# Kernel tuning notes

Measured on AMD Instinct MI355X. Metric: run time of the kernel, lower is better.

## Reference

```python
import jax, jax.numpy as jnp
import numpy as np

BATCH = 4096
N_AG = 32       # nodes (agents) per batch element
N_HE = 8        # hyperedges per batch element
F_IN = 256
F_OUT = 128
N_NODES = BATCH * N_AG
N_EDGES = BATCH * N_HE


def _build_incidence():
    # dense per-batch incidence (randn hyper_graph => all entries nonzero),
    # block-diagonal across the batch via index offsets
    b = jnp.arange(BATCH, dtype=jnp.int32)
    nodes = b[:, None, None] * N_AG + jnp.arange(N_AG, dtype=jnp.int32)[None, :, None]
    edges = b[:, None, None] * N_HE + jnp.arange(N_HE, dtype=jnp.int32)[None, None, :]
    node_idx = jnp.broadcast_to(nodes, (BATCH, N_AG, N_HE)).reshape(-1)
    edge_idx = jnp.broadcast_to(edges, (BATCH, N_AG, N_HE)).reshape(-1)
    return node_idx, edge_idx


def setup_inputs() -> dict:
    key = jax.random.key(0)
    k1, k2, k3 = jax.random.split(key, 3)
    inp = jax.random.normal(k1, (BATCH, N_AG, F_IN), jnp.float32)
    lin_w = jax.random.normal(k2, (F_IN, F_OUT), jnp.float32) * (1.0 / np.sqrt(F_IN))
    hgcn_bias = jnp.zeros((F_OUT,), jnp.float32)
    out_w = jax.random.normal(k3, (F_OUT, F_OUT), jnp.float32) * (1.0 / np.sqrt(F_OUT))
    out_b = jnp.zeros((F_OUT,), jnp.float32)
    node_idx, edge_idx = _build_incidence()
    return {"input": inp, "lin_w": lin_w, "hgcn_bias": hgcn_bias,
            "out_w": out_w, "out_b": out_b,
            "node_idx": node_idx, "edge_idx": edge_idx}


def reference(input, lin_w, hgcn_bias, out_w, out_b, node_idx, edge_idx):
    # X' = D^-1 H B^-1 H^T X Theta + bias, then Linear+ReLU output layer
    x = input.reshape(-1, F_IN) @ lin_w                       # [N, F_OUT]
    w = jnp.ones((N_EDGES,), x.dtype)                         # default hyperedge weights
    # node degree D (weighted by hyperedge weight) and edge degree B
    D = jax.ops.segment_sum(w[edge_idx], node_idx, num_segments=N_NODES)
    D_inv = jnp.where(D > 0, 1.0 / D, 0.0)
    deg = jax.ops.segment_sum(jnp.ones(edge_idx.shape, x.dtype), edge_idx,
                              num_segments=N_EDGES)
    B_inv = jnp.where(deg > 0, 1.0 / deg, 0.0)
    # propagate nodes -> hyperedges with norm B^-1 at target edges
    edge_feat = jax.ops.segment_sum(x[node_idx] * B_inv[edge_idx][:, None],
                                    edge_idx, num_segments=N_EDGES)   # [M, F_OUT]
    # propagate hyperedges -> nodes with norm D^-1 at target nodes
    out = jax.ops.segment_sum(edge_feat[edge_idx] * D_inv[node_idx][:, None],
                              node_idx, num_segments=N_NODES)         # [N, F_OUT]
    out = out + hgcn_bias
    return jax.nn.relu(out @ out_w + out_b)
```

## Files before the change

### kernel.cpp

```cpp
#include <hip/hip_runtime.h>


constexpr int BATCH = 4096;
constexpr int N_AG  = 32;
constexpr int F_IN  = 256;
constexpr int F_OUT = 128;
constexpr int G     = 8;

typedef float vfloat4 __attribute__((ext_vector_type(4)));
typedef float vfloat2 __attribute__((ext_vector_type(2)));

__global__ __launch_bounds__(512, 4) void hgcn_fused(
    const float* __restrict__ input,
    const float* __restrict__ lin_w,
    const float* __restrict__ bias1,
    const float* __restrict__ out_w,
    const float* __restrict__ bias2,
    float* __restrict__ out)
{
    const int t  = threadIdx.x;
    const int b0 = blockIdx.x * G;

    __shared__ __align__(16) float sm[G][F_IN];
    __shared__ __align__(16) float part[8][G][F_OUT];
    __shared__ __align__(16) float sh[G][F_OUT];
    __shared__ __align__(16) float sy[G][F_OUT];

    const int j2  = t & 63;
    const int oct = t >> 6;

    {
        const int g  = t >> 6;
        const int f4 = t & 63;
        const vfloat4* in4 = (const vfloat4*)input + (size_t)(b0 + g) * (N_AG * F_IN / 4);
        vfloat4 s = (vfloat4)0.f;
        #pragma unroll
        for (int a = 0; a < N_AG; ++a)
            s += __builtin_nontemporal_load(&in4[a * (F_IN / 4) + f4]);
        s *= (1.0f / 32.0f);
        *(vfloat4*)&sm[g][f4 * 4] = s;
    }
    __syncthreads();

    {
        const vfloat2* lw2 = (const vfloat2*)lin_w;
        const vfloat4* m4  = (const vfloat4*)&sm[0][0];
        vfloat2 acc[G];
        #pragma unroll
        for (int g = 0; g < G; ++g) acc[g] = (vfloat2)0.f;
        #pragma unroll 2
        for (int f4 = 0; f4 < 8; ++f4) {
            vfloat4 mm[G];
            #pragma unroll
            for (int g = 0; g < G; ++g)
                mm[g] = m4[g * (F_IN / 4) + oct * 8 + f4];
            #pragma unroll
            for (int c = 0; c < 4; ++c) {
                const int f = oct * 32 + f4 * 4 + c;
                vfloat2 wv = lw2[f * (F_OUT / 2) + j2];
                #pragma unroll
                for (int g = 0; g < G; ++g) {
                    acc[g].x += mm[g][c] * wv.x;
                    acc[g].y += mm[g][c] * wv.y;
                }
            }
        }
        #pragma unroll
        for (int g = 0; g < G; ++g)
            *(vfloat2*)&part[oct][g][j2 * 2] = acc[g];
    }
    __syncthreads();

    {
        const int g = t >> 6;
        const vfloat2* p2 = (const vfloat2*)&part[0][0][0];
        vfloat2 s = (vfloat2)0.f;
        #pragma unroll
        for (int o = 0; o < 8; ++o)
            s += p2[(o * G + g) * (F_OUT / 2) + j2];
        vfloat2 bb = ((const vfloat2*)bias1)[j2];
        s += bb;
        *(vfloat2*)&sh[g][j2 * 2] = s;
    }
    __syncthreads();

    {
        const vfloat2* ow2 = (const vfloat2*)out_w;
        const vfloat4* h4  = (const vfloat4*)&sh[0][0];
        vfloat2 acc[G];
        #pragma unroll
        for (int g = 0; g < G; ++g) acc[g] = (vfloat2)0.f;
        #pragma unroll 2
        for (int k4 = 0; k4 < 4; ++k4) {
            vfloat4 hh[G];
            #pragma unroll
            for (int g = 0; g < G; ++g)
                hh[g] = h4[g * (F_OUT / 4) + oct * 4 + k4];
            #pragma unroll
            for (int c = 0; c < 4; ++c) {
                const int k = oct * 16 + k4 * 4 + c;
                vfloat2 wv = ow2[k * (F_OUT / 2) + j2];
                #pragma unroll
                for (int g = 0; g < G; ++g) {
                    acc[g].x += hh[g][c] * wv.x;
                    acc[g].y += hh[g][c] * wv.y;
                }
            }
        }
        #pragma unroll
        for (int g = 0; g < G; ++g)
            *(vfloat2*)&part[oct][g][j2 * 2] = acc[g];
    }
    __syncthreads();

    {
        const int g = t >> 6;
        const vfloat2* p2 = (const vfloat2*)&part[0][0][0];
        vfloat2 s = (vfloat2)0.f;
        #pragma unroll
        for (int o = 0; o < 8; ++o)
            s += p2[(o * G + g) * (F_OUT / 2) + j2];
        vfloat2 bb = ((const vfloat2*)bias2)[j2];
        s += bb;
        vfloat2 yv;
        yv.x = s.x > 0.f ? s.x : 0.f;
        yv.y = s.y > 0.f ? s.y : 0.f;
        *(vfloat2*)&sy[g][j2 * 2] = yv;
    }
    __syncthreads();

    {
        const vfloat4* y4 = (const vfloat4*)&sy[0][0];
        const int col = t & 31;
        vfloat4 vy[G];
        #pragma unroll
        for (int g = 0; g < G; ++g) vy[g] = y4[g * 32 + col];
        vfloat4* o4 = (vfloat4*)out + (size_t)b0 * (N_AG * F_OUT / 4);
        #pragma unroll
        for (int r = 0; r < 16; ++r) {
            const int i = r * 512 + t;
            __builtin_nontemporal_store(vy[r >> 1], &o4[i]);
        }
    }
}

extern "C" void kernel_launch(void* const* d_in, const int* in_sizes, int n_in,
                              void* d_out, int out_size, void* d_ws, size_t ws_size,
                              hipStream_t stream) {
    const float* input = (const float*)d_in[0];
    const float* lin_w = (const float*)d_in[1];
    const float* b1    = (const float*)d_in[2];
    const float* out_w = (const float*)d_in[3];
    const float* b2    = (const float*)d_in[4];
    float* out = (float*)d_out;

    hgcn_fused<<<BATCH / G, 512, 0, stream>>>(input, lin_w, b1, out_w, b2, out);
}
```

Measured before the change: 214.8 us.

## Precompute fused weight matrix lin_w·out_w to collapse two GEMMs into one

A small pre-kernel multiplies lin_w by out_w, and folds bias1 through out_w and adds bias2, writing the product into workspace. The main kernel then runs one 256x128 matvec per group instead of two chained ones. This drops a stage, its barriers and the second weight read. The cost is an extra kernel launch each call, slightly different float rounding, and a fallback path that keeps the old kernel if workspace is too small.

```diff
diff --git a/kernel.cpp b/kernel.cpp
--- a/kernel.cpp
+++ b/kernel.cpp
@@ -10,24 +10,34 @@
 typedef float vfloat4 __attribute__((ext_vector_type(4)));
 typedef float vfloat2 __attribute__((ext_vector_type(2)));
 
-__global__ __launch_bounds__(512, 4) void hgcn_fused(
+__global__ __launch_bounds__(128) void fuse_weights(
+    const float* __restrict__ lin_w, const float* __restrict__ b1,
+    const float* __restrict__ out_w, const float* __restrict__ b2,
+    float* __restrict__ W, float* __restrict__ bf)
+{
+    const int j = threadIdx.x;
+    const int r = blockIdx.x;
+    const float* row = (r < F_IN) ? &lin_w[(size_t)r * F_OUT] : b1;
+    float acc = (r < F_IN) ? 0.f : b2[j];
+    #pragma unroll 8
+    for (int k = 0; k < F_OUT; ++k)
+        acc = fmaf(row[k], out_w[k * F_OUT + j], acc);
+    if (r < F_IN) W[r * F_OUT + j] = acc;
+    else          bf[j] = acc;
+}
+
+__global__ __launch_bounds__(512, 4) void hgcn_fusedw(
     const float* __restrict__ input,
-    const float* __restrict__ lin_w,
-    const float* __restrict__ bias1,
-    const float* __restrict__ out_w,
-    const float* __restrict__ bias2,
+    const float* __restrict__ W,
+    const float* __restrict__ bf,
     float* __restrict__ out)
 {
     const int t  = threadIdx.x;
     const int b0 = blockIdx.x * G;
 
     __shared__ __align__(16) float sm[G][F_IN];
-    __shared__ __align__(16) float part[8][G][F_OUT];
-    __shared__ __align__(16) float sh[G][F_OUT];
+    __shared__ __align__(16) float part[16][G][F_OUT];
     __shared__ __align__(16) float sy[G][F_OUT];
-
-    const int j2  = t & 63;
-    const int oct = t >> 6;
 
     {
         const int g  = t >> 6;
@@ -43,8 +53,87 @@
     __syncthreads();
 
     {
+        const int jq = t & 31, ks = t >> 5;
+        const vfloat4* W4 = (const vfloat4*)W;
+        const vfloat4* m4 = (const vfloat4*)&sm[0][0];
+        vfloat4 acc[G];
+        #pragma unroll
+        for (int g = 0; g < G; ++g) acc[g] = (vfloat4)0.f;
+        #pragma unroll
+        for (int f4 = 0; f4 < 4; ++f4) {
+            vfloat4 mm[G];
+            #pragma unroll
+            for (int g = 0; g < G; ++g)
+                mm[g] = m4[g * (F_IN / 4) + ks * 4 + f4];
+            #pragma unroll
+            for (int c = 0; c < 4; ++c) {
+                const int f = ks * 16 + f4 * 4 + c;
+                vfloat4 wv = W4[f * (F_OUT / 4) + jq];
+                #pragma unroll
+                for (int g = 0; g < G; ++g)
+                    acc[g] += mm[g][c] * wv;
+            }
+        }
+        #pragma unroll
+        for (int g = 0; g < G; ++g)
+            *(vfloat4*)&part[ks][g][jq * 4] = acc[g];
+    }
+    __syncthreads();
+
+    {
+        const int g = t >> 6, j2 = t & 63;
+        const vfloat2* p2 = (const vfloat2*)&part[0][0][0];
+        vfloat2 s = (vfloat2)0.f;
+        #pragma unroll
+        for (int ks = 0; ks < 16; ++ks)
+            s += p2[(ks * G + g) * (F_OUT / 2) + j2];
+        s += ((const vfloat2*)bf)[j2];
+        vfloat2 yv;
+        yv.x = s.x > 0.f ? s.x : 0.f;
+        yv.y = s.y > 0.f ? s.y : 0.f;
+        *(vfloat2*)&sy[g][j2 * 2] = yv;
+    }
+    __syncthreads();
+
+    {
+        const vfloat4* y4 = (const vfloat4*)&sy[0][0];
+        const int col = t & 31;
+        vfloat4 vy[G];
+        #pragma unroll
+        for (int g = 0; g < G; ++g) vy[g] = y4[g * 32 + col];
+        vfloat4* o4 = (vfloat4*)out + (size_t)b0 * (N_AG * F_OUT / 4);
+        #pragma unroll
+        for (int r = 0; r < 16; ++r)
+            __builtin_nontemporal_store(vy[r >> 1], &o4[r * 512 + t]);
+    }
+}
+
+__global__ __launch_bounds__(512, 4) void hgcn_fused_r3(
+    const float* __restrict__ input, const float* __restrict__ lin_w,
+    const float* __restrict__ bias1, const float* __restrict__ out_w,
+    const float* __restrict__ bias2, float* __restrict__ out)
+{
+    const int t = threadIdx.x;
+    const int b0 = blockIdx.x * G;
+    __shared__ __align__(16) float sm[G][F_IN];
+    __shared__ __align__(16) float part[8][G][F_OUT];
+    __shared__ __align__(16) float sh[G][F_OUT];
+    __shared__ __align__(16) float sy[G][F_OUT];
+    const int j2 = t & 63, oct = t >> 6;
+    {
+        const int g = t >> 6, f4 = t & 63;
+        const vfloat4* in4 = (const vfloat4*)input + (size_t)(b0 + g) * (N_AG * F_IN / 4);
+        vfloat4 s = (vfloat4)0.f;
+        #pragma unroll
+        for (int a = 0; a < N_AG; ++a)
+            s += __builtin_nontemporal_load(&in4[a * (F_IN / 4) + f4]);
+        s *= (1.0f / 32.0f);
+        *(vfloat4*)&sm[g][f4 * 4] = s;
+    }
+    __syncthreads();
+    {
         const vfloat2* lw2 = (const vfloat2*)lin_w;
-        const vfloat4* m4  = (const vfloat4*)&sm[0][0];
+        const vfloat4* m4 = (const vfloat4*)&sm[0][0];
         vfloat2 acc[G];
         #pragma unroll
         for (int g = 0; g < G; ++g) acc[g] = (vfloat2)0.f;
@@ -52,41 +141,33 @@
         for (int f4 = 0; f4 < 8; ++f4) {
             vfloat4 mm[G];
             #pragma unroll
-            for (int g = 0; g < G; ++g)
-                mm[g] = m4[g * (F_IN / 4) + oct * 8 + f4];
+            for (int g = 0; g < G; ++g) mm[g] = m4[g * (F_IN / 4) + oct * 8 + f4];
             #pragma unroll
             for (int c = 0; c < 4; ++c) {
-                const int f = oct * 32 + f4 * 4 + c;
-                vfloat2 wv = lw2[f * (F_OUT / 2) + j2];
+                vfloat2 wv = lw2[(oct * 32 + f4 * 4 + c) * (F_OUT / 2) + j2];
                 #pragma unroll
                 for (int g = 0; g < G; ++g) {
-                    acc[g].x += mm[g][c] * wv.x;
-                    acc[g].y += mm[g][c] * wv.y;
+                    acc[g].x += mm[g][c] * wv.x; acc[g].y += mm[g][c] * wv.y;
                 }
             }
         }
         #pragma unroll
-        for (int g = 0; g < G; ++g)
-            *(vfloat2*)&part[oct][g][j2 * 2] = acc[g];
-    }
-    __syncthreads();
-
+        for (int g = 0; g < G; ++g) *(vfloat2*)&part[oct][g][j2 * 2] = acc[g];
+    }
+    __syncthreads();
     {
         const int g = t >> 6;
         const vfloat2* p2 = (const vfloat2*)&part[0][0][0];
         vfloat2 s = (vfloat2)0.f;
         #pragma unroll
-        for (int o = 0; o < 8; ++o)
-            s += p2[(o * G + g) * (F_OUT / 2) + j2];
-        vfloat2 bb = ((const vfloat2*)bias1)[j2];
-        s += bb;
+        for (int o = 0; o < 8; ++o) s += p2[(o * G + g) * (F_OUT / 2) + j2];
+        s += ((const vfloat2*)bias1)[j2];
         *(vfloat2*)&sh[g][j2 * 2] = s;
     }
     __syncthreads();
-
     {
         const vfloat2* ow2 = (const vfloat2*)out_w;
-        const vfloat4* h4  = (const vfloat4*)&sh[0][0];
+        const vfloat4* h4 = (const vfloat4*)&sh[0][0];
         vfloat2 acc[G];
         #pragma unroll
         for (int g = 0; g < G; ++g) acc[g] = (vfloat2)0.f;
@@ -94,41 +175,33 @@
         for (int k4 = 0; k4 < 4; ++k4) {
             vfloat4 hh[G];
             #pragma unroll
-            for (int g = 0; g < G; ++g)
-                hh[g] = h4[g * (F_OUT / 4) + oct * 4 + k4];
+            for (int g = 0; g < G; ++g) hh[g] = h4[g * (F_OUT / 4) + oct * 4 + k4];
             #pragma unroll
             for (int c = 0; c < 4; ++c) {
-                const int k = oct * 16 + k4 * 4 + c;
-                vfloat2 wv = ow2[k * (F_OUT / 2) + j2];
+                vfloat2 wv = ow2[(oct * 16 + k4 * 4 + c) * (F_OUT / 2) + j2];
                 #pragma unroll
                 for (int g = 0; g < G; ++g) {
-                    acc[g].x += hh[g][c] * wv.x;
-                    acc[g].y += hh[g][c] * wv.y;
+                    acc[g].x += hh[g][c] * wv.x; acc[g].y += hh[g][c] * wv.y;
                 }
             }
         }
         #pragma unroll
-        for (int g = 0; g < G; ++g)
-            *(vfloat2*)&part[oct][g][j2 * 2] = acc[g];
-    }
-    __syncthreads();
-
+        for (int g = 0; g < G; ++g) *(vfloat2*)&part[oct][g][j2 * 2] = acc[g];
+    }
+    __syncthreads();
     {
         const int g = t >> 6;
         const vfloat2* p2 = (const vfloat2*)&part[0][0][0];
         vfloat2 s = (vfloat2)0.f;
         #pragma unroll
-        for (int o = 0; o < 8; ++o)
-            s += p2[(o * G + g) * (F_OUT / 2) + j2];
-        vfloat2 bb = ((const vfloat2*)bias2)[j2];
-        s += bb;
+        for (int o = 0; o < 8; ++o) s += p2[(o * G + g) * (F_OUT / 2) + j2];
+        s += ((const vfloat2*)bias2)[j2];
         vfloat2 yv;
         yv.x = s.x > 0.f ? s.x : 0.f;
         yv.y = s.y > 0.f ? s.y : 0.f;
         *(vfloat2*)&sy[g][j2 * 2] = yv;
     }
     __syncthreads();
-
     {
         const vfloat4* y4 = (const vfloat4*)&sy[0][0];
         const int col = t & 31;
@@ -137,10 +210,8 @@
         for (int g = 0; g < G; ++g) vy[g] = y4[g * 32 + col];
         vfloat4* o4 = (vfloat4*)out + (size_t)b0 * (N_AG * F_OUT / 4);
         #pragma unroll
-        for (int r = 0; r < 16; ++r) {
-            const int i = r * 512 + t;
-            __builtin_nontemporal_store(vy[r >> 1], &o4[i]);
-        }
+        for (int r = 0; r < 16; ++r)
+            __builtin_nontemporal_store(vy[r >> 1], &o4[r * 512 + t]);
     }
 }
 
@@ -154,5 +225,13 @@
     const float* b2    = (const float*)d_in[4];
     float* out = (float*)d_out;
 
-    hgcn_fused<<<BATCH / G, 512, 0, stream>>>(input, lin_w, b1, out_w, b2, out);
-}
+    const size_t need = (size_t)(F_IN * F_OUT + F_OUT) * sizeof(float);
+    if (ws_size >= need) {
+        float* W  = (float*)d_ws;
+        float* bf = W + F_IN * F_OUT;
+        fuse_weights<<<F_IN + 1, F_OUT, 0, stream>>>(lin_w, b1, out_w, b2, W, bf);
+        hgcn_fusedw<<<BATCH / G, 512, 0, stream>>>(input, W, bf, out);
+    } else {
+        hgcn_fused_r3<<<BATCH / G, 512, 0, stream>>>(input, lin_w, b1, out_w, b2, out);
+    }
+}
```

Result: slower. 221.3 us (+3.0%).

## Remove block barriers via wave-local reductions and prefetch weights into cache

Applied to the files above, without the earlier changes.

Reassigns the bias1 reduction and final output stage so each wave only reads data it wrote itself, replacing two __syncthreads with wave-local lgkmcnt waits. Each wave now writes the 32 output rows for its own batch element. It also issues early loads of lin_w and out_w to warm the cache while the input is being streamed. This cuts block-wide synchronisation and weight-load latency, at the cost of a few extra global loads and reliance on the LDS ordering within a wave.

```diff
diff --git a/kernel.cpp b/kernel.cpp
--- a/kernel.cpp
+++ b/kernel.cpp
@@ -18,28 +18,37 @@
     const float* __restrict__ bias2,
     float* __restrict__ out)
 {
-    const int t  = threadIdx.x;
-    const int b0 = blockIdx.x * G;
+    const int t    = threadIdx.x;
+    const int b0   = blockIdx.x * G;
+    const int wave = t >> 6;
+    const int lane = t & 63;
 
     __shared__ __align__(16) float sm[G][F_IN];
     __shared__ __align__(16) float part[8][G][F_OUT];
     __shared__ __align__(16) float sh[G][F_OUT];
     __shared__ __align__(16) float sy[G][F_OUT];
 
-    const int j2  = t & 63;
-    const int oct = t >> 6;
+    const int j2  = lane;
+    const int oct = wave;
+
+    float warm = 0.f;
+    {
+        #pragma unroll
+        for (int i = 0; i < 4; ++i) warm += lin_w[(t + 512 * i) * 16];
+        #pragma unroll
+        for (int i = 0; i < 2; ++i) warm += out_w[(t + 512 * i) * 16];
+    }
 
     {
-        const int g  = t >> 6;
-        const int f4 = t & 63;
-        const vfloat4* in4 = (const vfloat4*)input + (size_t)(b0 + g) * (N_AG * F_IN / 4);
+        const vfloat4* in4 = (const vfloat4*)input + (size_t)(b0 + wave) * (N_AG * F_IN / 4);
         vfloat4 s = (vfloat4)0.f;
         #pragma unroll
         for (int a = 0; a < N_AG; ++a)
-            s += __builtin_nontemporal_load(&in4[a * (F_IN / 4) + f4]);
+            s += __builtin_nontemporal_load(&in4[a * (F_IN / 4) + lane]);
         s *= (1.0f / 32.0f);
-        *(vfloat4*)&sm[g][f4 * 4] = s;
+        *(vfloat4*)&sm[wave][lane * 4] = s;
     }
+    asm volatile("" :: "v"(warm));
     __syncthreads();
 
     {
@@ -72,21 +81,19 @@
     __syncthreads();
 
     {
-        const int g = t >> 6;
-        const vfloat2* p2 = (const vfloat2*)&part[0][0][0];
-        vfloat2 s = (vfloat2)0.f;
-        #pragma unroll
-        for (int o = 0; o < 8; ++o)
-            s += p2[(o * G + g) * (F_OUT / 2) + j2];
-        vfloat2 bb = ((const vfloat2*)bias1)[j2];
-        s += bb;
-        *(vfloat2*)&sh[g][j2 * 2] = s;
-    }
-    __syncthreads();
+        {
+            const int g  = lane >> 3;
+            const int kk = oct * 16 + (lane & 7) * 2;
+            vfloat2 s = (vfloat2)0.f;
+            #pragma unroll
+            for (int o = 0; o < 8; ++o)
+                s += *(const vfloat2*)&part[o][g][kk];
+            s += *(const vfloat2*)&bias1[kk];
+            *(vfloat2*)&sh[g][kk] = s;
+        }
+        asm volatile("s_waitcnt lgkmcnt(0)" ::: "memory");
 
-    {
         const vfloat2* ow2 = (const vfloat2*)out_w;
-        const vfloat4* h4  = (const vfloat4*)&sh[0][0];
         vfloat2 acc[G];
         #pragma unroll
         for (int g = 0; g < G; ++g) acc[g] = (vfloat2)0.f;
@@ -95,7 +102,7 @@
             vfloat4 hh[G];
             #pragma unroll
             for (int g = 0; g < G; ++g)
-                hh[g] = h4[g * (F_OUT / 4) + oct * 4 + k4];
+                hh[g] = *(const vfloat4*)&sh[g][oct * 16 + k4 * 4];
             #pragma unroll
             for (int c = 0; c < 4; ++c) {
                 const int k = oct * 16 + k4 * 4 + c;
@@ -114,32 +121,26 @@
     __syncthreads();
 
     {
-        const int g = t >> 6;
-        const vfloat2* p2 = (const vfloat2*)&part[0][0][0];
+        const int g = wave;
         vfloat2 s = (vfloat2)0.f;
         #pragma unroll
         for (int o = 0; o < 8; ++o)
-            s += p2[(o * G + g) * (F_OUT / 2) + j2];
-        vfloat2 bb = ((const vfloat2*)bias2)[j2];
-        s += bb;
+            s += *(const vfloat2*)&part[o][g][j2 * 2];
+        s += ((const vfloat2*)bias2)[j2];
         vfloat2 yv;
         yv.x = s.x > 0.f ? s.x : 0.f;
         yv.y = s.y > 0.f ? s.y : 0.f;
         *(vfloat2*)&sy[g][j2 * 2] = yv;
-    }
-    __syncthreads();
+        asm volatile("s_waitcnt lgkmcnt(0)" ::: "memory");
 
-    {
-        const vfloat4* y4 = (const vfloat4*)&sy[0][0];
-        const int col = t & 31;
-        vfloat4 vy[G];
-        #pragma unroll
-        for (int g = 0; g < G; ++g) vy[g] = y4[g * 32 + col];
-        vfloat4* o4 = (vfloat4*)out + (size_t)b0 * (N_AG * F_OUT / 4);
+        const int col = lane & 31;
+        const int rh  = lane >> 5;
+        const vfloat4 vy = ((const vfloat4*)&sy[g][0])[col];
+        vfloat4* o4 = (vfloat4*)out + ((size_t)(b0 + g) * N_AG) * (F_OUT / 4);
         #pragma unroll
         for (int r = 0; r < 16; ++r) {
-            const int i = r * 512 + t;
-            __builtin_nontemporal_store(vy[r >> 1], &o4[i]);
+            const int row = r * 2 + rh;
+            __builtin_nontemporal_store(vy, &o4[row * (F_OUT / 4) + col]);
         }
     }
 }
```

Measured after the change: 213.7 us (median of 2 runs). No clear change (-0.5%).
